# Kernel tuning notes

Measured on AMD Instinct MI355X. Metric: run time of the kernel, lower is better.

Reference implementation:

```python
import jax, jax.numpy as jnp
import numpy as np

FEAT = 1433
HID = 2
NUM_CLASS = 7
EPS = 1e-5  # torch BatchNorm1d default eps


def _bn_softsign(h, gamma, beta):
    # BatchNorm1d in training mode: batch stats over (batch, length) per channel.
    mu = h.mean(axis=(0, 2), keepdims=True)
    var = h.var(axis=(0, 2), keepdims=True)  # biased, matches torch normalization
    hn = (h - mu) * jax.lax.rsqrt(var + EPS)
    hn = hn * gamma[None, :, None] + beta[None, :, None]
    return hn / (1.0 + jnp.abs(hn))  # Softsign


def feature_adjacency(x, y):
    # (x.unsqueeze(-1) * y.unsqueeze(-2)).sum(dim=1) with x channel dim == 1
    # reduces to an outer product of x[:,0] with neighbor.sum over K.
    adj = jnp.einsum('bf,bg->bfg', x.sum(1), y.sum(1))  # [B,F,F]
    adj = adj + jnp.swapaxes(adj, -1, -2)
    adj = jnp.sqrt(adj)
    # row_normalize: divide by sum over dim 1, zero out inf/nan
    norm = adj / adj.sum(axis=1, keepdims=True)
    norm = jnp.where(jnp.isfinite(norm), norm, 0.0)
    return norm + jnp.eye(FEAT, dtype=x.dtype)


def featbrd(x, adj, W, b):
    # adjacency-based feature conv: y[b,c,f] = sum_g adj[(b),f,g] x[b,c,g],
    # then 1x1 conv over channels (Conv1d kernel_size=1).
    if adj.shape[0] == 1:
        y = jnp.einsum('fg,bcg->bcf', adj[0], x)
    else:
        y = jnp.einsum('bfg,bcg->bcf', adj, x)
    return jnp.einsum('oc,bcf->bof', W, y) + b[None, :, None]


def setup_inputs() -> dict:
    key = jax.random.key(0)
    ks = jax.random.split(key, 10)
    B, K = 64, 8
    inp = {
        'x': jax.random.uniform(ks[0], (B, 1, FEAT), dtype=jnp.float32),
        'neighbor': jax.random.uniform(ks[1], (B, K, FEAT), dtype=jnp.float32),
        'adj_buf': jnp.zeros((1, FEAT, FEAT), jnp.float32),
        'W1': jax.random.normal(ks[2], (HID, 1), jnp.float32) * 0.5,
        'b1': jnp.zeros((HID,), jnp.float32),
        'W2': jax.random.normal(ks[3], (HID, HID), jnp.float32) * 0.5,
        'b2': jnp.zeros((HID,), jnp.float32),
        'g1': jnp.ones((HID,), jnp.float32),
        'be1': jnp.zeros((HID,), jnp.float32),
        'g2': jnp.ones((HID,), jnp.float32),
        'be2': jnp.zeros((HID,), jnp.float32),
        'Wc': jax.random.normal(ks[4], (NUM_CLASS, FEAT * HID), jnp.float32) * 0.02,
        'bc': jnp.zeros((NUM_CLASS,), jnp.float32),
    }
    return inp


def reference(x, neighbor, adj_buf, W1, b1, W2, b2, g1, be1, g2, be2, Wc, bc):
    fadj = feature_adjacency(x, neighbor)          # [B,F,F]
    adj_tot = adj_buf + fadj.sum(0)                # [1,F,F] (buffer starts at zero)
    h = _bn_softsign(featbrd(x, fadj, W1, b1), g1, be1)      # [B,HID,F]
    h = _bn_softsign(featbrd(h, adj_tot, W2, b2), g2, be2)   # [B,HID,F]
    flat = h.reshape(h.shape[0], -1)               # Flatten (C then F, row-major)
    return flat @ Wc.T + bc
```

## Files before the change

kernel.cpp:

```cpp
#include <hip/hip_runtime.h>
#include <hip/hip_bf16.h>
#include <math.h>

constexpr int F   = 1433;
constexpr int NB  = 64;
constexpr int KN  = 8;
constexpr int BF  = NB * F;
constexpr float EPS = 1e-5f;

constexpr int SF  = 32;
constexpr int CH  = (F + SF - 1) / SF;
constexpr int AbS = 1440;
constexpr int SK  = 15;
constexpr int KCH = 96;
constexpr int FT  = 8;
constexpr int NAB = 6 * 180;
constexpr int NST = 256;

constexpr int O_YS  = 0;
constexpr int O_DP  = O_YS + BF;
constexpr int O_Y1P = O_DP + SF * BF;
constexpr int O_P   = O_Y1P + SF * BF;
constexpr int O_Y1  = O_P + 4 * BF;
constexpr int O_Y2  = O_Y1 + BF;
constexpr int O_G2P = O_Y2 + 2 * BF;
constexpr int O_AB  = O_G2P + SK * 128 * F;
constexpr int O_ST  = O_AB + (F * AbS) / 2;

__global__ __launch_bounds__(256) void k_D(const float* __restrict__ x,
                                           const float* __restrict__ nbr,
                                           float* __restrict__ DP,
                                           float* __restrict__ ys_out) {
  __shared__ __align__(16) float2 xy[F];
  const int b = blockIdx.x, s = blockIdx.y;
  for (int i = threadIdx.x; i < F; i += 256) {
    const float* p = nbr + (size_t)b * KN * F + i;
    float acc = 0.f;
#pragma unroll
    for (int k = 0; k < KN; ++k) acc += p[k * F];
    xy[i] = make_float2(x[b * F + i], acc);
  }
  __syncthreads();
  if (s == 0) {
    for (int i = threadIdx.x; i < F; i += 256) ys_out[b * F + i] = xy[i].y;
  }
  const int cs = s * CH, cn = min(CH, F - cs);
  float gx[6], gy[6], acc[6] = {};
#pragma unroll
  for (int j = 0; j < 6; ++j) {
    int g = threadIdx.x + 256 * j;
    float2 p = (g < F) ? xy[g] : make_float2(0.f, 0.f);
    gx[j] = p.x; gy[j] = p.y;
  }
#pragma unroll 5
  for (int i = 0; i < cn; ++i) {
    float2 p = xy[cs + i];
#pragma unroll
    for (int j = 0; j < 6; ++j)
      acc[j] += __builtin_amdgcn_sqrtf(fmaf(gy[j], p.x, gx[j] * p.y));
  }
#pragma unroll
  for (int j = 0; j < 6; ++j) {
    int g = threadIdx.x + 256 * j;
    if (g < F) DP[(size_t)s * BF + b * F + g] = acc[j];
  }
}

__global__ __launch_bounds__(256) void k_y1(const float* __restrict__ x,
                                            const float* __restrict__ ys,
                                            const float* __restrict__ DP,
                                            float* __restrict__ Y1P,
                                            float4* __restrict__ P) {
  __shared__ __align__(16) float4 pl[CH];
  const int b = blockIdx.x, s = blockIdx.y;
  const int cs = s * CH, cn = min(CH, F - cs);
  for (int i = threadIdx.x; i < cn; i += 256) {
    int g = cs + i;
    float d = 0.f;
#pragma unroll
    for (int t = 0; t < SF; ++t) d += DP[(size_t)t * BF + b * F + g];
    float inv = (d > 0.f) ? 1.f / d : 0.f;
    float xv = x[b * F + g], yv = ys[b * F + g];
    float4 pv = make_float4(xv, yv, xv * inv, inv);
    pl[i] = pv;
    P[b * F + g] = pv;
  }
  __syncthreads();
  float fx[6], fy[6], acc[6] = {};
#pragma unroll
  for (int j = 0; j < 6; ++j) {
    int f = threadIdx.x + 256 * j;
    fx[j] = (f < F) ? x[b * F + f] : 0.f;
    fy[j] = (f < F) ? ys[b * F + f] : 0.f;
  }
#pragma unroll 5
  for (int i = 0; i < cn; ++i) {
    float4 p = pl[i];
#pragma unroll
    for (int j = 0; j < 6; ++j)
      acc[j] = fmaf(__builtin_amdgcn_sqrtf(fmaf(fx[j], p.y, fy[j] * p.x)), p.z, acc[j]);
  }
#pragma unroll
  for (int j = 0; j < 6; ++j) {
    int f = threadIdx.x + 256 * j;
    if (f < F) Y1P[(size_t)s * BF + b * F + f] = acc[j];
  }
}

__global__ __launch_bounds__(256) void k_Astats(const float* __restrict__ x,
                                                const float* __restrict__ ys,
                                                const float4* __restrict__ P,
                                                const float* __restrict__ Y1P,
                                                __hip_bfloat16* __restrict__ Ab,
                                                float* __restrict__ y1,
                                                float* __restrict__ st) {
  const int bid = blockIdx.x;
  if (bid < NAB) {
    __shared__ float2 fxy[FT][NB];
    const int gx = bid % 6, fy = bid / 6;
    const int fbase = fy * FT;
    for (int i = threadIdx.x; i < FT * NB; i += 256) {
      int b = i >> 3, j = i & 7;
      int f = fbase + j;
      float vx = 0.f, vy = 0.f;
      if (f < F) { vx = x[b * F + f]; vy = ys[b * F + f]; }
      fxy[j][b] = make_float2(vx, vy);
    }
    __syncthreads();
    const int g = gx * 256 + threadIdx.x;
    if (g >= AbS) return;
    if (g < F) {
      float acc[FT] = {};
      float4 pc = P[g];
#pragma unroll 2
      for (int b = 0; b < NB; ++b) {
        float4 pn;
        if (b < NB - 1) pn = P[(b + 1) * F + g];
#pragma unroll
        for (int j = 0; j < FT; ++j) {
          float2 w = fxy[j][b];
          acc[j] = fmaf(__builtin_amdgcn_sqrtf(fmaf(w.x, pc.y, pc.x * w.y)), pc.w, acc[j]);
        }
        pc = pn;
      }
#pragma unroll
      for (int j = 0; j < FT; ++j) {
        int f = fbase + j;
        if (f < F) Ab[(size_t)f * AbS + g] = __float2bfloat16(acc[j]);
      }
    } else {
#pragma unroll
      for (int j = 0; j < FT; ++j) {
        int f = fbase + j;
        if (f < F) Ab[(size_t)f * AbS + g] = __float2bfloat16(0.f);
      }
    }
  } else {
    const int sid = bid - NAB;
    float s = 0.f, sq = 0.f;
    for (int i = sid * 256 + threadIdx.x; i < BF; i += NST * 256) {
      float v = x[i];
#pragma unroll
      for (int k = 0; k < SF; ++k) v += Y1P[(size_t)k * BF + i];
      y1[i] = v;
      s += v; sq += v * v;
    }
#pragma unroll
    for (int o = 32; o; o >>= 1) {
      s += __shfl_down(s, o, 64);
      sq += __shfl_down(sq, o, 64);
    }
    __shared__ float ls[4], lq[4];
    int wave = threadIdx.x >> 6, lane = threadIdx.x & 63;
    if (lane == 0) { ls[wave] = s; lq[wave] = sq; }
    __syncthreads();
    if (threadIdx.x == 0) {
      atomicAdd(&st[0], ls[0] + ls[1] + ls[2] + ls[3]);
      atomicAdd(&st[1], lq[0] + lq[1] + lq[2] + lq[3]);
    }
  }
}

struct GP { uint2 a; float yv[8]; };

__global__ __launch_bounds__(256) void k_gemm(const ushort* __restrict__ Ab,
                                              const float* __restrict__ y1,
                                              const float* __restrict__ st,
                                              const float* __restrict__ W1,
                                              const float* __restrict__ g1,
                                              const float* __restrict__ be1,
                                              float* __restrict__ G2P) {
  const float mu = st[0] / (float)BF;
  const float var = st[1] / (float)BF - mu * mu;
  const float wa = W1[0], wb = W1[1];
  const float k0 = wa * g1[0] / sqrtf(wa * wa * var + EPS);
  const float k1 = wb * g1[1] / sqrtf(wb * wb * var + EPS);
  const float c0 = -k0 * mu + be1[0];
  const float c1 = -k1 * mu + be1[1];

  __shared__ __align__(16) float Al[2][32 * 36];
  __shared__ __align__(16) float Hl[2][32 * 132];
  const int f0 = blockIdx.x * 32;
  const int gs = blockIdx.y * KCH;
  const int tid = threadIdx.x;
  const int ffs = tid >> 3;
  const int g4s = (tid & 7) * 4;
  const int hb = tid & 7;
  const int hg = tid >> 3;
  const int fsub = (tid & 7) * 4;
  const int msub = (tid >> 3) * 4;

  auto loadRegs = [&](int gb, GP& p) {
    const int f = f0 + ffs;
    p.a = make_uint2(0u, 0u);
    if (f < F) p.a = *(const uint2*)&Ab[(size_t)f * AbS + gb + g4s];
    const int gl = min(gb + hg, F - 1);
#pragma unroll
    for (int r = 0; r < 8; ++r) p.yv[r] = y1[(hb + 8 * r) * F + gl];
  };
  auto storeLDS = [&](int buf, const GP& p) {
    Al[buf][(g4s + 0) * 36 + ffs] = __uint_as_float(p.a.x << 16);
    Al[buf][(g4s + 1) * 36 + ffs] = __uint_as_float(p.a.x & 0xffff0000u);
    Al[buf][(g4s + 2) * 36 + ffs] = __uint_as_float(p.a.y << 16);
    Al[buf][(g4s + 3) * 36 + ffs] = __uint_as_float(p.a.y & 0xffff0000u);
#pragma unroll
    for (int r = 0; r < 8; ++r) {
      const int b = hb + 8 * r;
      const float v = p.yv[r];
      float h0 = fmaf(k0, v, c0); h0 = h0 / (1.f + fabsf(h0));
      float h1 = fmaf(k1, v, c1); h1 = h1 / (1.f + fabsf(h1));
      *(float2*)&Hl[buf][hg * 132 + 2 * b] = make_float2(h0, h1);
    }
  };

  float acc[4][4] = {};
  GP p;
  loadRegs(gs, p);
  storeLDS(0, p);
  __syncthreads();

  for (int c = 0; c < 3; ++c) {
    const int buf = c & 1;
    GP pn;
    if (c < 2) loadRegs(gs + (c + 1) * 32, pn);
    const float* Ab_ = Al[buf];
    const float* Hb_ = Hl[buf];
#pragma unroll 4
    for (int gi = 0; gi < 32; ++gi) {
      float4 a4 = *(const float4*)&Ab_[gi * 36 + fsub];
      float4 h4 = *(const float4*)&Hb_[gi * 132 + msub];
      float av[4] = {a4.x, a4.y, a4.z, a4.w};
      float hv[4] = {h4.x, h4.y, h4.z, h4.w};
#pragma unroll
      for (int i = 0; i < 4; ++i)
#pragma unroll
        for (int j = 0; j < 4; ++j)
          acc[i][j] = fmaf(av[i], hv[j], acc[i][j]);
    }
    if (c < 2) storeLDS(buf ^ 1, pn);
    __syncthreads();
  }

  float* dst = G2P + (size_t)blockIdx.y * 128 * F;
#pragma unroll
  for (int i = 0; i < 4; ++i) {
    int f = f0 + fsub + i;
    if (f < F) {
#pragma unroll
      for (int j = 0; j < 4; ++j)
        dst[(msub + j) * F + f] = acc[i][j];
    }
  }
}

__global__ __launch_bounds__(256) void k_stats2(const float* __restrict__ y1,
                                                const float* __restrict__ G2P,
                                                const float* __restrict__ st,
                                                const float* __restrict__ W1,
                                                const float* __restrict__ g1,
                                                const float* __restrict__ be1,
                                                float* __restrict__ y2,
                                                float* __restrict__ stw) {
  const float mu = st[0] / (float)BF;
  const float var = st[1] / (float)BF - mu * mu;
  const float wa = W1[0], wb = W1[1];
  const float k0 = wa * g1[0] / sqrtf(wa * wa * var + EPS);
  const float k1 = wb * g1[1] / sqrtf(wb * wb * var + EPS);
  const float c0 = -k0 * mu + be1[0];
  const float c1 = -k1 * mu + be1[1];

  float su = 0.f, sv = 0.f, suu = 0.f, svv = 0.f, suv = 0.f;
  for (int i = blockIdx.x * 256 + threadIdx.x; i < BF; i += gridDim.x * 256) {
    int b = i / F, f = i - b * F;
    float w = y1[i];
    float h0 = fmaf(k0, w, c0); h0 = h0 / (1.f + fabsf(h0));
    float h1 = fmaf(k1, w, c1); h1 = h1 / (1.f + fabsf(h1));
    int iu = (2 * b) * F + f, iv = iu + F;
    float u = 64.f * h0, v = 64.f * h1;
#pragma unroll
    for (int s = 0; s < SK; ++s) {
      u += G2P[(size_t)s * 128 * F + iu];
      v += G2P[(size_t)s * 128 * F + iv];
    }
    y2[iu] = u; y2[iv] = v;
    su += u; sv += v; suu += u * u; svv += v * v; suv += u * v;
  }
#pragma unroll
  for (int o = 32; o; o >>= 1) {
    su += __shfl_down(su, o, 64);
    sv += __shfl_down(sv, o, 64);
    suu += __shfl_down(suu, o, 64);
    svv += __shfl_down(svv, o, 64);
    suv += __shfl_down(suv, o, 64);
  }
  __shared__ float red[5][4];
  int wave = threadIdx.x >> 6, lane = threadIdx.x & 63;
  if (lane == 0) {
    red[0][wave] = su; red[1][wave] = sv; red[2][wave] = suu;
    red[3][wave] = svv; red[4][wave] = suv;
  }
  __syncthreads();
  if (threadIdx.x == 0) {
    atomicAdd(&stw[2], red[0][0] + red[0][1] + red[0][2] + red[0][3]);
    atomicAdd(&stw[3], red[1][0] + red[1][1] + red[1][2] + red[1][3]);
    atomicAdd(&stw[4], red[2][0] + red[2][1] + red[2][2] + red[2][3]);
    atomicAdd(&stw[5], red[3][0] + red[3][1] + red[3][2] + red[3][3]);
    atomicAdd(&stw[6], red[4][0] + red[4][1] + red[4][2] + red[4][3]);
  }
}

__global__ __launch_bounds__(256) void k_out(const float* __restrict__ y2,
                                             const float* __restrict__ st,
                                             const float* __restrict__ W2,
                                             const float* __restrict__ b2,
                                             const float* __restrict__ g2,
                                             const float* __restrict__ be2,
                                             const float* __restrict__ Wc,
                                             const float* __restrict__ bc,
                                             float* __restrict__ out) {
  float n = (float)BF;
  float Eu = st[2] / n, Ev = st[3] / n;
  float Euu = st[4] / n, Evv = st[5] / n, Euv = st[6] / n;
  float cA[2], cB[2], cC[2];
#pragma unroll
  for (int o = 0; o < 2; ++o) {
    float w0 = W2[o * 2 + 0], w1 = W2[o * 2 + 1];
    float mean = w0 * Eu + w1 * Ev + b2[o];
    float Eh2 = w0 * w0 * Euu + 2.f * w0 * w1 * Euv + w1 * w1 * Evv +
                2.f * b2[o] * (w0 * Eu + w1 * Ev) + b2[o] * b2[o];
    float var = Eh2 - mean * mean;
    float inv = g2[o] / sqrtf(var + EPS);
    cA[o] = w0 * inv;
    cB[o] = w1 * inv;
    cC[o] = (b2[o] - mean) * inv + be2[o];
  }
  const int b = blockIdx.x;
  float acc[7] = {};
  for (int f = threadIdx.x; f < F; f += 256) {
    float u = y2[(2 * b) * F + f], v = y2[(2 * b + 1) * F + f];
    float h0 = fmaf(cA[0], u, fmaf(cB[0], v, cC[0]));
    h0 = h0 / (1.f + fabsf(h0));
    float h1 = fmaf(cA[1], u, fmaf(cB[1], v, cC[1]));
    h1 = h1 / (1.f + fabsf(h1));
#pragma unroll
    for (int o = 0; o < 7; ++o) acc[o] = fmaf(Wc[o * (2 * F) + f], h0, acc[o]);
#pragma unroll
    for (int o = 0; o < 7; ++o) acc[o] = fmaf(Wc[o * (2 * F) + F + f], h1, acc[o]);
  }
#pragma unroll
  for (int o = 0; o < 7; ++o) {
#pragma unroll
    for (int s = 32; s; s >>= 1) acc[o] += __shfl_down(acc[o], s, 64);
  }
  __shared__ float red[7][4];
  int wave = threadIdx.x >> 6, lane = threadIdx.x & 63;
  if (lane == 0) {
#pragma unroll
    for (int o = 0; o < 7; ++o) red[o][wave] = acc[o];
  }
  __syncthreads();
  if (threadIdx.x < 7) {
    int o = threadIdx.x;
    out[b * 7 + o] = red[o][0] + red[o][1] + red[o][2] + red[o][3] + bc[o];
  }
}

extern "C" void kernel_launch(void* const* d_in, const int* in_sizes, int n_in,
                              void* d_out, int out_size, void* d_ws, size_t ws_size,
                              hipStream_t stream) {
  const float* x    = (const float*)d_in[0];
  const float* nbr  = (const float*)d_in[1];
  const float* W1   = (const float*)d_in[3];
  const float* W2   = (const float*)d_in[5];
  const float* b2   = (const float*)d_in[6];
  const float* g1   = (const float*)d_in[7];
  const float* be1  = (const float*)d_in[8];
  const float* g2   = (const float*)d_in[9];
  const float* be2  = (const float*)d_in[10];
  const float* Wc   = (const float*)d_in[11];
  const float* bc   = (const float*)d_in[12];
  float* out = (float*)d_out;
  float* ws = (float*)d_ws;

  float*  ys  = ws + O_YS;
  float*  DP  = ws + O_DP;
  float*  Y1P = ws + O_Y1P;
  float4* P   = (float4*)(ws + O_P);
  float*  y1  = ws + O_Y1;
  float*  y2  = ws + O_Y2;
  float*  G2P = ws + O_G2P;
  __hip_bfloat16* Ab = (__hip_bfloat16*)(ws + O_AB);
  float*  st  = ws + O_ST;

  hipMemsetAsync(st, 0, 64 * sizeof(float), stream);

  k_D     <<<dim3(NB, SF), 256, 0, stream>>>(x, nbr, DP, ys);
  k_y1    <<<dim3(NB, SF), 256, 0, stream>>>(x, ys, DP, Y1P, P);
  k_Astats<<<NAB + NST, 256, 0, stream>>>(x, ys, P, Y1P, Ab, y1, st);
  k_gemm  <<<dim3(45, SK), 256, 0, stream>>>((const ushort*)Ab, y1, st, W1, g1, be1, G2P);
  k_stats2<<<NST, 256, 0, stream>>>(y1, G2P, st, W1, g1, be1, y2, st);
  k_out   <<<NB, 256, 0, stream>>>(y2, st, W2, b2, g2, be2, Wc, bc, out);
}
```

Baseline: 209.5 us.

## Hoist neighbor sum into separate kernel, halve column splits, widen A-tile rows

Adds a k_ys kernel that computes the neighbor sum once and zeroes the stats buffer, which replaces the memset and the 32-fold redundant neighbor reduction that every k_D block did before. k_D now stages only its own chunk in shared memory and reads its per-thread values from global memory. The column split count drops from 32 to 16, so each block handles a larger chunk and the partial-sum buffers are half as large. k_Astats processes 12 feature rows per block instead of 8, giving 720 blocks instead of 1080. The trade-off is one extra launch and less parallelism in the D and y1 stages.

```diff
diff --git a/kernel.cpp b/kernel.cpp
--- a/kernel.cpp
+++ b/kernel.cpp
@@ -8,13 +8,12 @@
 constexpr int BF  = NB * F;
 constexpr float EPS = 1e-5f;
 
-constexpr int SF  = 32;
-constexpr int CH  = (F + SF - 1) / SF;
+constexpr int SF  = 16;
+constexpr int CH  = 90;
 constexpr int AbS = 1440;
 constexpr int SK  = 15;
-constexpr int KCH = 96;
-constexpr int FT  = 8;
-constexpr int NAB = 6 * 180;
+constexpr int FT  = 12;
+constexpr int NA  = 720;
 constexpr int NST = 256;
 
 constexpr int O_YS  = 0;
@@ -27,34 +26,39 @@
 constexpr int O_AB  = O_G2P + SK * 128 * F;
 constexpr int O_ST  = O_AB + (F * AbS) / 2;
 
+__global__ __launch_bounds__(256) void k_ys(const float* __restrict__ nbr,
+                                            float* __restrict__ ys,
+                                            float* __restrict__ st) {
+  if (blockIdx.x == 0 && threadIdx.x < 64) st[threadIdx.x] = 0.f;
+  int i = blockIdx.x * 256 + threadIdx.x;
+  if (i >= BF) return;
+  int b = i / F, g = i - b * F;
+  const float* p = nbr + (size_t)b * KN * F + g;
+  float s = 0.f;
+#pragma unroll
+  for (int k = 0; k < KN; ++k) s += p[k * F];
+  ys[i] = s;
+}
+
 __global__ __launch_bounds__(256) void k_D(const float* __restrict__ x,
-                                           const float* __restrict__ nbr,
-                                           float* __restrict__ DP,
-                                           float* __restrict__ ys_out) {
-  __shared__ __align__(16) float2 xy[F];
+                                           const float* __restrict__ ys,
+                                           float* __restrict__ DP) {
+  __shared__ __align__(8) float2 xyc[CH];
   const int b = blockIdx.x, s = blockIdx.y;
-  for (int i = threadIdx.x; i < F; i += 256) {
-    const float* p = nbr + (size_t)b * KN * F + i;
-    float acc = 0.f;
-#pragma unroll
-    for (int k = 0; k < KN; ++k) acc += p[k * F];
-    xy[i] = make_float2(x[b * F + i], acc);
-  }
+  const int cs = s * CH, cn = min(CH, F - cs);
+  for (int i = threadIdx.x; i < cn; i += 256)
+    xyc[i] = make_float2(x[b * F + cs + i], ys[b * F + cs + i]);
   __syncthreads();
-  if (s == 0) {
-    for (int i = threadIdx.x; i < F; i += 256) ys_out[b * F + i] = xy[i].y;
-  }
-  const int cs = s * CH, cn = min(CH, F - cs);
   float gx[6], gy[6], acc[6] = {};
 #pragma unroll
   for (int j = 0; j < 6; ++j) {
     int g = threadIdx.x + 256 * j;
-    float2 p = (g < F) ? xy[g] : make_float2(0.f, 0.f);
-    gx[j] = p.x; gy[j] = p.y;
-  }
-#pragma unroll 5
+    gx[j] = (g < F) ? x[b * F + g] : 0.f;
+    gy[j] = (g < F) ? ys[b * F + g] : 0.f;
+  }
+#pragma unroll 6
   for (int i = 0; i < cn; ++i) {
-    float2 p = xy[cs + i];
+    float2 p = xyc[i];
 #pragma unroll
     for (int j = 0; j < 6; ++j)
       acc[j] += __builtin_amdgcn_sqrtf(fmaf(gy[j], p.x, gx[j] * p.y));
@@ -93,7 +97,7 @@
     fx[j] = (f < F) ? x[b * F + f] : 0.f;
     fy[j] = (f < F) ? ys[b * F + f] : 0.f;
   }
-#pragma unroll 5
+#pragma unroll 6
   for (int i = 0; i < cn; ++i) {
     float4 p = pl[i];
 #pragma unroll
@@ -115,30 +119,32 @@
                                                 float* __restrict__ y1,
                                                 float* __restrict__ st) {
   const int bid = blockIdx.x;
-  if (bid < NAB) {
+  if (bid < NA) {
     __shared__ float2 fxy[FT][NB];
-    const int gx = bid % 6, fy = bid / 6;
+    const int gxc = bid % 6, fy = bid / 6;
     const int fbase = fy * FT;
-    for (int i = threadIdx.x; i < FT * NB; i += 256) {
-      int b = i >> 3, j = i & 7;
+#pragma unroll
+    for (int r = 0; r < 3; ++r) {
+      int i = threadIdx.x + 256 * r;
+      int j = i >> 6, bb = i & 63;
       int f = fbase + j;
       float vx = 0.f, vy = 0.f;
-      if (f < F) { vx = x[b * F + f]; vy = ys[b * F + f]; }
-      fxy[j][b] = make_float2(vx, vy);
+      if (f < F) { vx = x[bb * F + f]; vy = ys[bb * F + f]; }
+      fxy[j][bb] = make_float2(vx, vy);
     }
     __syncthreads();
-    const int g = gx * 256 + threadIdx.x;
+    const int g = gxc * 256 + threadIdx.x;
     if (g >= AbS) return;
     if (g < F) {
       float acc[FT] = {};
       float4 pc = P[g];
 #pragma unroll 2
-      for (int b = 0; b < NB; ++b) {
-        float4 pn;
-        if (b < NB - 1) pn = P[(b + 1) * F + g];
+      for (int bb = 0; bb < NB; ++bb) {
+        float4 pn = pc;
+        if (bb < NB - 1) pn = P[(bb + 1) * F + g];
 #pragma unroll
         for (int j = 0; j < FT; ++j) {
-          float2 w = fxy[j][b];
+          float2 w = fxy[j][bb];
           acc[j] = fmaf(__builtin_amdgcn_sqrtf(fmaf(w.x, pc.y, pc.x * w.y)), pc.w, acc[j]);
         }
         pc = pn;
@@ -156,23 +162,23 @@
       }
     }
   } else {
-    const int sid = bid - NAB;
-    float s = 0.f, sq = 0.f;
+    const int sid = bid - NA;
+    float sv = 0.f, sq = 0.f;
     for (int i = sid * 256 + threadIdx.x; i < BF; i += NST * 256) {
       float v = x[i];
 #pragma unroll
-      for (int k = 0; k < SF; ++k) v += Y1P[(size_t)k * BF + i];
+      for (int t = 0; t < SF; ++t) v += Y1P[(size_t)t * BF + i];
       y1[i] = v;
-      s += v; sq += v * v;
+      sv += v; sq += v * v;
     }
 #pragma unroll
     for (int o = 32; o; o >>= 1) {
-      s += __shfl_down(s, o, 64);
+      sv += __shfl_down(sv, o, 64);
       sq += __shfl_down(sq, o, 64);
     }
     __shared__ float ls[4], lq[4];
     int wave = threadIdx.x >> 6, lane = threadIdx.x & 63;
-    if (lane == 0) { ls[wave] = s; lq[wave] = sq; }
+    if (lane == 0) { ls[wave] = sv; lq[wave] = sq; }
     __syncthreads();
     if (threadIdx.x == 0) {
       atomicAdd(&st[0], ls[0] + ls[1] + ls[2] + ls[3]);
@@ -180,8 +186,6 @@
     }
   }
 }
-
-struct GP { uint2 a; float yv[8]; };
 
 __global__ __launch_bounds__(256) void k_gemm(const ushort* __restrict__ Ab,
                                               const float* __restrict__ y1,
@@ -201,54 +205,49 @@
   __shared__ __align__(16) float Al[2][32 * 36];
   __shared__ __align__(16) float Hl[2][32 * 132];
   const int f0 = blockIdx.x * 32;
-  const int gs = blockIdx.y * KCH;
+  const int gs = blockIdx.y * 96;
   const int tid = threadIdx.x;
-  const int ffs = tid >> 3;
-  const int g4s = (tid & 7) * 4;
-  const int hb = tid & 7;
-  const int hg = tid >> 3;
-  const int fsub = (tid & 7) * 4;
-  const int msub = (tid >> 3) * 4;
-
-  auto loadRegs = [&](int gb, GP& p) {
+  const int ffs = tid >> 3, g4s = (tid & 7) * 4;
+  const int hb = tid & 7, hg = tid >> 3;
+  const int fsub = (tid & 7) * 4, msub = (tid >> 3) * 4;
+
+  uint2 pa; float pyv[8];
+  auto loadRegs = [&](int gb) {
     const int f = f0 + ffs;
-    p.a = make_uint2(0u, 0u);
-    if (f < F) p.a = *(const uint2*)&Ab[(size_t)f * AbS + gb + g4s];
+    pa = make_uint2(0u, 0u);
+    if (f < F) pa = *(const uint2*)&Ab[(size_t)f * AbS + gb + g4s];
     const int gl = min(gb + hg, F - 1);
 #pragma unroll
-    for (int r = 0; r < 8; ++r) p.yv[r] = y1[(hb + 8 * r) * F + gl];
+    for (int r = 0; r < 8; ++r) pyv[r] = y1[(hb + 8 * r) * F + gl];
   };
-  auto storeLDS = [&](int buf, const GP& p) {
-    Al[buf][(g4s + 0) * 36 + ffs] = __uint_as_float(p.a.x << 16);
-    Al[buf][(g4s + 1) * 36 + ffs] = __uint_as_float(p.a.x & 0xffff0000u);
-    Al[buf][(g4s + 2) * 36 + ffs] = __uint_as_float(p.a.y << 16);
-    Al[buf][(g4s + 3) * 36 + ffs] = __uint_as_float(p.a.y & 0xffff0000u);
+  auto storeLDS = [&](int buf) {
+    Al[buf][(g4s + 0) * 36 + ffs] = __uint_as_float(pa.x << 16);
+    Al[buf][(g4s + 1) * 36 + ffs] = __uint_as_float(pa.x & 0xffff0000u);
+    Al[buf][(g4s + 2) * 36 + ffs] = __uint_as_float(pa.y << 16);
+    Al[buf][(g4s + 3) * 36 + ffs] = __uint_as_float(pa.y & 0xffff0000u);
 #pragma unroll
     for (int r = 0; r < 8; ++r) {
-      const int b = hb + 8 * r;
-      const float v = p.yv[r];
+      const int bb = hb + 8 * r;
+      const float v = pyv[r];
       float h0 = fmaf(k0, v, c0); h0 = h0 / (1.f + fabsf(h0));
       float h1 = fmaf(k1, v, c1); h1 = h1 / (1.f + fabsf(h1));
-      *(float2*)&Hl[buf][hg * 132 + 2 * b] = make_float2(h0, h1);
+      *(float2*)&Hl[buf][hg * 132 + 2 * bb] = make_float2(h0, h1);
     }
   };
 
   float acc[4][4] = {};
-  GP p;
-  loadRegs(gs, p);
-  storeLDS(0, p);
+  loadRegs(gs);
+  storeLDS(0);
   __syncthreads();
-
   for (int c = 0; c < 3; ++c) {
     const int buf = c & 1;
-    GP pn;
-    if (c < 2) loadRegs(gs + (c + 1) * 32, pn);
-    const float* Ab_ = Al[buf];
-    const float* Hb_ = Hl[buf];
+    if (c < 2) loadRegs(gs + (c + 1) * 32);
+    const float* A_ = Al[buf];
+    const float* H_ = Hl[buf];
 #pragma unroll 4
     for (int gi = 0; gi < 32; ++gi) {
-      float4 a4 = *(const float4*)&Ab_[gi * 36 + fsub];
-      float4 h4 = *(const float4*)&Hb_[gi * 132 + msub];
+      float4 a4 = *(const float4*)&A_[gi * 36 + fsub];
+      float4 h4 = *(const float4*)&H_[gi * 132 + msub];
       float av[4] = {a4.x, a4.y, a4.z, a4.w};
       float hv[4] = {h4.x, h4.y, h4.z, h4.w};
 #pragma unroll
@@ -257,10 +256,9 @@
         for (int j = 0; j < 4; ++j)
           acc[i][j] = fmaf(av[i], hv[j], acc[i][j]);
     }
-    if (c < 2) storeLDS(buf ^ 1, pn);
+    if (c < 2) storeLDS(buf ^ 1);
     __syncthreads();
   }
-
   float* dst = G2P + (size_t)blockIdx.y * 128 * F;
 #pragma unroll
   for (int i = 0; i < 4; ++i) {
@@ -298,9 +296,9 @@
     int iu = (2 * b) * F + f, iv = iu + F;
     float u = 64.f * h0, v = 64.f * h1;
 #pragma unroll
-    for (int s = 0; s < SK; ++s) {
-      u += G2P[(size_t)s * 128 * F + iu];
-      v += G2P[(size_t)s * 128 * F + iv];
+    for (int t = 0; t < SK; ++t) {
+      u += G2P[(size_t)t * 128 * F + iu];
+      v += G2P[(size_t)t * 128 * F + iv];
     }
     y2[iu] = u; y2[iv] = v;
     su += u; sv += v; suu += u * u; svv += v * v; suv += u * v;
@@ -321,11 +319,9 @@
   }
   __syncthreads();
   if (threadIdx.x == 0) {
-    atomicAdd(&stw[2], red[0][0] + red[0][1] + red[0][2] + red[0][3]);
-    atomicAdd(&stw[3], red[1][0] + red[1][1] + red[1][2] + red[1][3]);
-    atomicAdd(&stw[4], red[2][0] + red[2][1] + red[2][2] + red[2][3]);
-    atomicAdd(&stw[5], red[3][0] + red[3][1] + red[3][2] + red[3][3]);
-    atomicAdd(&stw[6], red[4][0] + red[4][1] + red[4][2] + red[4][3]);
+#pragma unroll
+    for (int m = 0; m < 5; ++m)
+      atomicAdd(&stw[2 + m], red[m][0] + red[m][1] + red[m][2] + red[m][3]);
   }
 }
 
@@ -348,8 +344,8 @@
     float mean = w0 * Eu + w1 * Ev + b2[o];
     float Eh2 = w0 * w0 * Euu + 2.f * w0 * w1 * Euv + w1 * w1 * Evv +
                 2.f * b2[o] * (w0 * Eu + w1 * Ev) + b2[o] * b2[o];
-    float var = Eh2 - mean * mean;
-    float inv = g2[o] / sqrtf(var + EPS);
+    float vr = Eh2 - mean * mean;
+    float inv = g2[o] / sqrtf(vr + EPS);
     cA[o] = w0 * inv;
     cB[o] = w1 * inv;
     cC[o] = (b2[o] - mean) * inv + be2[o];
@@ -400,7 +396,7 @@
   const float* Wc   = (const float*)d_in[11];
   const float* bc   = (const float*)d_in[12];
   float* out = (float*)d_out;
-  float* ws = (float*)d_ws;
+  float* ws  = (float*)d_ws;
 
   float*  ys  = ws + O_YS;
   float*  DP  = ws + O_DP;
@@ -412,11 +408,10 @@
   __hip_bfloat16* Ab = (__hip_bfloat16*)(ws + O_AB);
   float*  st  = ws + O_ST;
 
-  hipMemsetAsync(st, 0, 64 * sizeof(float), stream);
-
-  k_D     <<<dim3(NB, SF), 256, 0, stream>>>(x, nbr, DP, ys);
+  k_ys    <<<(BF + 255) / 256, 256, 0, stream>>>(nbr, ys, st);
+  k_D     <<<dim3(NB, SF), 256, 0, stream>>>(x, ys, DP);
   k_y1    <<<dim3(NB, SF), 256, 0, stream>>>(x, ys, DP, Y1P, P);
-  k_Astats<<<NAB + NST, 256, 0, stream>>>(x, ys, P, Y1P, Ab, y1, st);
+  k_Astats<<<NA + NST, 256, 0, stream>>>(x, ys, P, Y1P, Ab, y1, st);
   k_gemm  <<<dim3(45, SK), 256, 0, stream>>>((const ushort*)Ab, y1, st, W1, g1, be1, G2P);
   k_stats2<<<NST, 256, 0, stream>>>(y1, G2P, st, W1, g1, be1, y2, st);
   k_out   <<<NB, 256, 0, stream>>>(y2, st, W2, b2, g2, be2, Wc, bc, out);
```

Result: no change. 208.2 us (-0.6%).
